# Performance work log

Hardware: AMD Instinct MI355X
Metric: run time of the kernel (lower is better)

The kernel has to match this reference:

```python
import jax, jax.numpy as jnp
import numpy as np

N = 50000      # num nodes
E = 800000     # num edges (before self loops)
B = 50         # num graphs in batch
F_IN = 15
C = 64         # hidden_channels
H = 4          # num_heads
NEG_SLOPE = 0.2  # PyG GATConv default


def setup_inputs() -> dict:
    key = jax.random.key(0)
    ks = jax.random.split(key, 32)
    s = 0.05
    inp = {
        "x": jax.random.normal(ks[0], (N, F_IN), dtype=jnp.float32),
        "edge_index": jax.random.randint(ks[1], (2, E), 0, N, dtype=jnp.int32),
        "batch": jnp.sort(jax.random.randint(ks[2], (N,), 0, B, dtype=jnp.int32)),
        "W1": jax.random.normal(ks[3], (F_IN, H * C)) * s,
        "aS1": jax.random.normal(ks[4], (H, C)) * s,
        "aD1": jax.random.normal(ks[5], (H, C)) * s,
        "b1": jnp.zeros((H * C,)),
        "W2": jax.random.normal(ks[6], (H * C, H * C)) * s,
        "aS2": jax.random.normal(ks[7], (H, C)) * s,
        "aD2": jax.random.normal(ks[8], (H, C)) * s,
        "b2": jnp.zeros((H * C,)),
        # GAT layer 3: 256 -> 64, 1 head
        "W3": jax.random.normal(ks[9], (H * C, C)) * s,
        "aS3": jax.random.normal(ks[10], (1, C)) * s,
        "aD3": jax.random.normal(ks[11], (1, C)) * s,
        "b3": jnp.zeros((C,)),
        # node attention MLP: 64 -> 32 -> 1
        "Wna1": jax.random.normal(ks[12], (C, 32)) * s,
        "bna1": jnp.zeros((32,)),
        "Wna2": jax.random.normal(ks[13], (32, 1)) * s,
        "bna2": jnp.zeros((1,)),
        # graph classifier: 128 -> 128 -> 64 -> 1
        "Wc1": jax.random.normal(ks[14], (2 * C, 128)) * s,
        "bc1": jnp.zeros((128,)),
        "Wc2": jax.random.normal(ks[15], (128, 64)) * s,
        "bc2": jnp.zeros((64,)),
        "Wc3": jax.random.normal(ks[16], (64, 1)) * s,
        "bc3": jnp.zeros((1,)),
    }
    return inp


def _gat_conv(x, src, dst, W, a_src, a_dst, b, heads, ch):
    """PyG-style GATConv (add_self_loops=True, negative_slope=0.2, eval mode)."""
    n = x.shape[0]
    h = (x @ W).reshape(n, heads, ch)               # [N, H, C]
    alpha_s = jnp.einsum('nhc,hc->nh', h, a_src)    # per-node src score
    alpha_d = jnp.einsum('nhc,hc->nh', h, a_dst)
    loops = jnp.arange(n, dtype=src.dtype)
    s = jnp.concatenate([src, loops])               # [E+N]
    d = jnp.concatenate([dst, loops])
    e = jax.nn.leaky_relu(alpha_s[s] + alpha_d[d], NEG_SLOPE)   # [E+N, H]
    # segment softmax over incoming edges of each dst node
    m = jax.ops.segment_max(e, d, num_segments=n)
    ex = jnp.exp(e - m[d])
    denom = jax.ops.segment_sum(ex, d, num_segments=n)
    alpha = ex / denom[d]                           # [E+N, H]
    msg = h[s] * alpha[:, :, None]                  # [E+N, H, C]
    out = jax.ops.segment_sum(msg, d, num_segments=n)  # [N, H, C]
    return out.reshape(n, heads * ch) + b


def reference(x, edge_index, batch, W1, aS1, aD1, b1, W2, aS2, aD2, b2,
              W3, aS3, aD3, b3, Wna1, bna1, Wna2, bna2,
              Wc1, bc1, Wc2, bc2, Wc3, bc3):
    src, dst = edge_index[0], edge_index[1]
    x1 = jax.nn.elu(_gat_conv(x, src, dst, W1, aS1, aD1, b1, H, C))
    x2 = jax.nn.elu(_gat_conv(x1, src, dst, W2, aS2, aD2, b2, H, C))
    x3 = jax.nn.elu(_gat_conv(x2, src, dst, W3, aS3, aD3, b3, 1, C))  # [N, 64]

    # node attention: MLP then softmax over ALL nodes (dim=0, as in source)
    na = jax.nn.relu(x3 @ Wna1 + bna1) @ Wna2 + bna2   # [N, 1]
    node_attention = jax.nn.softmax(na, axis=0)

    # graph pooling
    ones = jnp.ones((x3.shape[0],), dtype=x3.dtype)
    cnt = jax.ops.segment_sum(ones, batch, num_segments=B)         # [B]
    mean = jax.ops.segment_sum(x3, batch, num_segments=B) / jnp.maximum(cnt, 1.0)[:, None]
    mx = jax.ops.segment_max(x3, batch, num_segments=B)
    mx = jnp.where(cnt[:, None] > 0, mx, 0.0)
    g = jnp.concatenate([mean, mx], axis=1)                        # [B, 128]

    h1 = jax.nn.relu(g @ Wc1 + bc1)
    h2 = jax.nn.relu(h1 @ Wc2 + bc2)
    risk = jax.nn.sigmoid(h2 @ Wc3 + bc3)                          # [B, 1]
    return (risk, node_attention)
```

## Files before the change

### kernel.cpp

```cpp
#include <hip/hip_runtime.h>
#include <math.h>

#define NN 50000
#define NP 50176
#define EE 800000
#define ETOT (EE + NN)
#define BB 50
#define PC 16

typedef unsigned short u16;
typedef unsigned char u8;
typedef __attribute__((ext_vector_type(8))) short short8;
typedef __attribute__((ext_vector_type(4))) float floatx4;
typedef __attribute__((ext_vector_type(2))) float floatx2;

__device__ __forceinline__ float b2f(u16 u) {
  return __int_as_float(((int)u) << 16);
}
__device__ __forceinline__ u16 f2b(float f) {
  unsigned u = __float_as_uint(f);
  unsigned r = (u + 0x7fffu + ((u >> 16) & 1u)) >> 16;
  return (u16)r;
}
__device__ __forceinline__ u8 f2f8(float v) {
  return (u8)(__builtin_amdgcn_cvt_pk_fp8_f32(v, v, 0, false) & 0xFF);
}
__device__ __forceinline__ float readlane_f(float v, int l) {
  return __int_as_float(__builtin_amdgcn_readlane(__float_as_int(v), l));
}

__global__ void count_kernel(const int* __restrict__ ei, int* __restrict__ cnt) {
  int e = blockIdx.x * blockDim.x + threadIdx.x;
  if (e >= ETOT) return;
  int d = (e < EE) ? ei[EE + e] : (e - EE);
  atomicAdd(&cnt[d], 1);
}

__global__ void scan1_kernel(const int* __restrict__ cnt, int* __restrict__ rowp,
                             int* __restrict__ part) {
  __shared__ int s[512];
  int t = threadIdx.x;
  int i = blockIdx.x * 512 + t;
  int v = (i < NN) ? cnt[i] : 0;
  s[t] = v;
  __syncthreads();
  for (int off = 1; off < 512; off <<= 1) {
    int add = (t >= off) ? s[t - off] : 0;
    __syncthreads();
    s[t] += add;
    __syncthreads();
  }
  if (i < NN) rowp[i] = s[t] - v;
  if (t == 511) part[blockIdx.x] = s[511];
}

__global__ void scan2_kernel(int* __restrict__ part, int* __restrict__ rowp) {
  __shared__ int s[128];
  int t = threadIdx.x;
  int v = (t < 98) ? part[t] : 0;
  s[t] = v;
  __syncthreads();
  for (int off = 1; off < 128; off <<= 1) {
    int add = (t >= off) ? s[t - off] : 0;
    __syncthreads();
    s[t] += add;
    __syncthreads();
  }
  if (t < 98) part[t] = s[t] - v;
  if (t == 97) rowp[NN] = s[97];
}

__global__ void scan3_kernel(int* __restrict__ rowp, const int* __restrict__ part) {
  int i = blockIdx.x * 512 + threadIdx.x;
  if (i < NN) rowp[i] += part[blockIdx.x];
}

__global__ void fill_kernel(const int* __restrict__ ei, const int* __restrict__ rowp,
                            int* __restrict__ cur, int* __restrict__ col) {
  int e = blockIdx.x * blockDim.x + threadIdx.x;
  if (e >= ETOT) return;
  int s, d;
  if (e < EE) { s = ei[e]; d = ei[EE + e]; } else { s = e - EE; d = s; }
  int p = atomicAdd(&cur[d], 1);
  col[rowp[d] + p] = s;
}

__global__ void prep_kernel(const float* __restrict__ x, const float* __restrict__ W1,
                            const float* __restrict__ W2, const float* __restrict__ W3,
                            u16* __restrict__ xb, u16* __restrict__ W1t,
                            u16* __restrict__ W2t, u16* __restrict__ W3t) {
  const int T0 = NP * 32, T1 = T0 + 8192, T2 = T1 + 65536, T3 = T2 + 16384;
  int i = blockIdx.x * 256 + threadIdx.x;
  if (i < T0) {
    int n = i >> 5, c = i & 31;
    xb[i] = (n < NN && c < 15) ? f2b(x[n * 15 + c]) : (u16)0;
  } else if (i < T1) {
    int j = i - T0, n = j >> 5, k = j & 31;
    W1t[j] = (k < 15) ? f2b(W1[k * 256 + n]) : (u16)0;
  } else if (i < T2) {
    int j = i - T1, n = j >> 8, k = j & 255;
    W2t[j] = f2b(W2[k * 256 + n]);
  } else if (i < T3) {
    int j = i - T2, n = j >> 8, k = j & 255;
    W3t[j] = f2b(W3[k * 64 + n]);
  }
}

template <int BK, bool F8>
__global__ __launch_bounds__(256) void gemm_bf16_kernel(
    const u16* __restrict__ A, const u16* __restrict__ Bt, u16* __restrict__ C,
    u8* __restrict__ C8, int K, int N, const float* __restrict__ aS,
    const float* __restrict__ aD, float* __restrict__ as_o,
    float* __restrict__ ad_o, int Hh) {
  __shared__ u16 Al[128][BK + 8];
  __shared__ u16 Bl[64][BK + 8];
  __shared__ float sS[4][64], sD[4][64];
  int R0 = blockIdx.x * 128, C0 = blockIdx.y * 64;
  int wid = threadIdx.x >> 6, lane = threadIdx.x & 63;
  int wr = (wid >> 1) * 64, wc = (wid & 1) * 32;
  int lrow = lane & 15, lk8 = (lane >> 4) * 8;
  int rq = (lane >> 4) * 4;
  const int Q4 = BK / 4;
  const int nA = 128 * Q4, nB = 64 * Q4;
  floatx4 acc[4][2];
#pragma unroll
  for (int i = 0; i < 4; ++i)
#pragma unroll
    for (int j = 0; j < 2; ++j) acc[i][j] = (floatx4){0.f, 0.f, 0.f, 0.f};

  for (int k0 = 0; k0 < K; k0 += BK) {
    for (int c = threadIdx.x; c < nA + nB; c += 256) {
      if (c < nA) {
        int r = c / Q4, o = (c % Q4) * 4;
        *(ushort4*)&Al[r][o] = *(const ushort4*)&A[(size_t)(R0 + r) * K + k0 + o];
      } else {
        int c2 = c - nA;
        int r = c2 / Q4, o = (c2 % Q4) * 4;
        *(ushort4*)&Bl[r][o] = *(const ushort4*)&Bt[(size_t)(C0 + r) * K + k0 + o];
      }
    }
    __syncthreads();
#pragma unroll
    for (int ks = 0; ks < BK / 32; ++ks) {
      short8 a[4], b[2];
#pragma unroll
      for (int i = 0; i < 4; ++i) a[i] = *(const short8*)&Al[wr + i * 16 + lrow][ks * 32 + lk8];
#pragma unroll
      for (int j = 0; j < 2; ++j) b[j] = *(const short8*)&Bl[wc + j * 16 + lrow][ks * 32 + lk8];
#pragma unroll
      for (int i = 0; i < 4; ++i)
#pragma unroll
        for (int j = 0; j < 2; ++j)
          acc[i][j] = __builtin_amdgcn_mfma_f32_16x16x32_bf16(a[i], b[j], acc[i][j], 0, 0, 0);
    }
    __syncthreads();
  }
#pragma unroll
  for (int i = 0; i < 4; ++i)
#pragma unroll
    for (int j = 0; j < 2; ++j)
#pragma unroll
      for (int q = 0; q < 4; ++q) {
        int gr = R0 + wr + i * 16 + rq + q;
        int gc = C0 + wc + j * 16 + lrow;
        if constexpr (F8)
          C8[(size_t)gr * N + gc] = f2f8(acc[i][j][q]);
        else
          C[(size_t)gr * N + gc] = f2b(acc[i][j][q]);
      }
  int hb = blockIdx.y * 64;
  float wS0 = aS[hb + wc + lrow], wS1 = aS[hb + wc + 16 + lrow];
  float wD0 = aD[hb + wc + lrow], wD1 = aD[hb + wc + 16 + lrow];
#pragma unroll
  for (int i = 0; i < 4; ++i)
#pragma unroll
    for (int q = 0; q < 4; ++q) {
      float vS = acc[i][0][q] * wS0 + acc[i][1][q] * wS1;
      float vD = acc[i][0][q] * wD0 + acc[i][1][q] * wD1;
#pragma unroll
      for (int o = 8; o; o >>= 1) {
        vS += __shfl_xor(vS, o, 64);
        vD += __shfl_xor(vD, o, 64);
      }
      if (lrow == 0) {
        int rl = i * 16 + rq + q;
        sS[wid][rl] = vS;
        sD[wid][rl] = vD;
      }
    }
  __syncthreads();
  if (threadIdx.x < 128) {
    int p = threadIdx.x >> 6, r = threadIdx.x & 63;
    int gr = R0 + p * 64 + r;
    as_o[(size_t)gr * Hh + blockIdx.y] = sS[2 * p][r] + sS[2 * p + 1][r];
    ad_o[(size_t)gr * Hh + blockIdx.y] = sD[2 * p][r] + sD[2 * p + 1][r];
  }
}

template <int B>
__device__ __forceinline__ void agg4_batch(
    const u8* __restrict__ h8, int s, int kbase, int cnt, int hj, int lq,
    const float (*__restrict__ exsw)[4], float& a0, float& a1, float& a2, float& a3) {
  unsigned wv[B];
  float qv[B];
#pragma unroll
  for (int u = 0; u < B; ++u) {
    int ke = kbase + u;
    int kc = (ke < cnt) ? ke : (cnt - 1);
    int sk = __builtin_amdgcn_readlane(s, kc);
    qv[u] = (ke < cnt) ? exsw[kc][hj] : 0.f;
    wv[u] = *(const unsigned*)&h8[(size_t)sk * 256 + lq];
  }
#pragma unroll
  for (int u = 0; u < B; ++u) {
    floatx2 lo = __builtin_amdgcn_cvt_pk_f32_fp8(wv[u], false);
    floatx2 hi = __builtin_amdgcn_cvt_pk_f32_fp8(wv[u], true);
    a0 += qv[u] * lo.x;
    a1 += qv[u] * lo.y;
    a2 += qv[u] * hi.x;
    a3 += qv[u] * hi.y;
  }
}

__global__ __launch_bounds__(256) void agg4_kernel(
    const u8* __restrict__ h8, const float* __restrict__ as_i,
    const float* __restrict__ ad_i, const int* __restrict__ rowp,
    const int* __restrict__ col, const float* __restrict__ bias,
    u16* __restrict__ xo) {
  __shared__ float exs[4][64][4];
  int wid = threadIdx.x >> 6, lane = threadIdx.x & 63;
  int d = blockIdx.x * 4 + wid;
  int rp0 = rowp[d], deg = rowp[d + 1] - rp0;
  float4 add = *(const float4*)&ad_i[(size_t)d * 4];
  int hj = lane >> 4;
  int lq = lane << 2;
  const float(*exsw)[4] = exs[wid];
  float a0 = 0.f, a1 = 0.f, a2 = 0.f, a3 = 0.f;
  float den0 = 0.f, den1 = 0.f, den2 = 0.f, den3 = 0.f;

  for (int base = 0; base < deg; base += 64) {
    int i = base + lane;
    bool valid = i < deg;
    int s = valid ? col[rp0 + i] : 0;
    float4 asv = *(const float4*)&as_i[(size_t)s * 4];
    float e0 = asv.x + add.x, e1 = asv.y + add.y, e2 = asv.z + add.z, e3 = asv.w + add.w;
    e0 = (e0 > 0.f) ? e0 : 0.2f * e0;
    e1 = (e1 > 0.f) ? e1 : 0.2f * e1;
    e2 = (e2 > 0.f) ? e2 : 0.2f * e2;
    e3 = (e3 > 0.f) ? e3 : 0.2f * e3;
    float x0 = valid ? __expf(e0) : 0.f;
    float x1 = valid ? __expf(e1) : 0.f;
    float x2 = valid ? __expf(e2) : 0.f;
    float x3 = valid ? __expf(e3) : 0.f;
    den0 += x0; den1 += x1; den2 += x2; den3 += x3;
    *(float4*)&exs[wid][lane][0] = make_float4(x0, x1, x2, x3);
    __threadfence_block();
    int cnt = min(64, deg - base);
    for (int kb = 0; kb < cnt; kb += 16)
      agg4_batch<16>(h8, s, kb, cnt, hj, lq, exsw, a0, a1, a2, a3);
  }
#pragma unroll
  for (int o = 32; o; o >>= 1) {
    den0 += __shfl_xor(den0, o, 64);
    den1 += __shfl_xor(den1, o, 64);
    den2 += __shfl_xor(den2, o, 64);
    den3 += __shfl_xor(den3, o, 64);
  }
  float den = (hj == 0) ? den0 : (hj == 1) ? den1 : (hj == 2) ? den2 : den3;
  float inv = 1.f / den;
  float4 bv = *(const float4*)&bias[lq];
  float v0 = a0 * inv + bv.x;
  float v1 = a1 * inv + bv.y;
  float v2 = a2 * inv + bv.z;
  float v3 = a3 * inv + bv.w;
  v0 = (v0 > 0.f) ? v0 : expm1f(v0);
  v1 = (v1 > 0.f) ? v1 : expm1f(v1);
  v2 = (v2 > 0.f) ? v2 : expm1f(v2);
  v3 = (v3 > 0.f) ? v3 : expm1f(v3);
  ushort4 o4;
  o4.x = f2b(v0); o4.y = f2b(v1); o4.z = f2b(v2); o4.w = f2b(v3);
  ((ushort4*)xo)[(size_t)d * 64 + lane] = o4;
}

__global__ __launch_bounds__(256) void agg1na_kernel(
    const u16* __restrict__ h, const float* __restrict__ as_i,
    const float* __restrict__ ad_i, const int* __restrict__ rowp,
    const int* __restrict__ col, const float* __restrict__ bias,
    float* __restrict__ xo, const float* __restrict__ Wna1,
    const float* __restrict__ bna1, const float* __restrict__ Wna2,
    const float* __restrict__ bna2, float* __restrict__ na) {
  __shared__ float Ws[2048];
  __shared__ float W2s[32];
  __shared__ float xrow[4][64];
  for (int i = threadIdx.x; i < 2048; i += 256) Ws[i] = Wna1[i];
  if (threadIdx.x < 32) W2s[threadIdx.x] = Wna2[threadIdx.x];
  __syncthreads();
  int wid = threadIdx.x >> 6, lane = threadIdx.x & 63;
  int d = blockIdx.x * 4 + wid;
  int rp0 = rowp[d], deg = rowp[d + 1] - rp0;
  float add = ad_i[d];
  float acc = 0.f, den = 0.f;
  for (int base = 0; base < deg; base += 64) {
    int i = base + lane;
    bool valid = i < deg;
    int s = valid ? col[rp0 + i] : 0;
    float e = as_i[s] + add;
    e = (e > 0.f) ? e : 0.2f * e;
    float ex = valid ? __expf(e) : 0.f;
    den += ex;
    int cnt = min(64, deg - base);
    int k8 = cnt & ~7;
    for (int k = 0; k < k8; k += 8) {
      int sA[8];
      float qA[8], hv[8];
#pragma unroll
      for (int u = 0; u < 8; ++u) {
        sA[u] = __builtin_amdgcn_readlane(s, k + u);
        qA[u] = readlane_f(ex, k + u);
      }
#pragma unroll
      for (int u = 0; u < 8; ++u) hv[u] = b2f(h[(size_t)sA[u] * 64 + lane]);
      float p0 = qA[0] * hv[0] + qA[1] * hv[1];
      float p1 = qA[2] * hv[2] + qA[3] * hv[3];
      float p2 = qA[4] * hv[4] + qA[5] * hv[5];
      float p3 = qA[6] * hv[6] + qA[7] * hv[7];
      acc += (p0 + p1) + (p2 + p3);
    }
    for (int k = k8; k < cnt; ++k) {
      int sk = __builtin_amdgcn_readlane(s, k);
      float qk = readlane_f(ex, k);
      acc += qk * b2f(h[(size_t)sk * 64 + lane]);
    }
  }
#pragma unroll
  for (int o = 32; o; o >>= 1) den += __shfl_xor(den, o, 64);
  float v = acc / den + bias[lane];
  v = (v > 0.f) ? v : expm1f(v);
  xo[(size_t)d * 64 + lane] = v;
  xrow[wid][lane] = v;
  __threadfence_block();
  int j = lane & 31;
  int coff = (lane >> 5) * 32;
  float hj = 0.f;
#pragma unroll
  for (int c = 0; c < 32; ++c) hj += xrow[wid][coff + c] * Ws[(coff + c) * 32 + j];
  hj += __shfl_xor(hj, 32, 64);
  hj += bna1[j];
  float r = fmaxf(hj, 0.f) * W2s[j];
#pragma unroll
  for (int o = 16; o; o >>= 1) r += __shfl_xor(r, o, 64);
  if (lane == 0) na[d] = __expf(r + bna2[0]);
}

__global__ void na_sum_kernel(const float* __restrict__ na, float* __restrict__ gsum) {
  __shared__ float s[4];
  float acc = 0.f;
  for (int i = blockIdx.x * blockDim.x + threadIdx.x; i < NN; i += gridDim.x * blockDim.x)
    acc += na[i];
  for (int o = 32; o; o >>= 1) acc += __shfl_xor(acc, o, 64);
  int wid = threadIdx.x >> 6, lane = threadIdx.x & 63;
  if (lane == 0) s[wid] = acc;
  __syncthreads();
  if (threadIdx.x == 0) atomicAdd(gsum, s[0] + s[1] + s[2] + s[3]);
}

__global__ void na_write_kernel(const float* __restrict__ na, const float* __restrict__ gsum,
                                float* __restrict__ out) {
  int n = blockIdx.x * blockDim.x + threadIdx.x;
  if (n >= NN) return;
  out[n] = na[n] / gsum[0];
}

__global__ void pool1_kernel(const float* __restrict__ x3, const int* __restrict__ batch,
                             float* __restrict__ ppsum, float* __restrict__ ppmax) {
  int b = blockIdx.x, c = blockIdx.y;
  int lane = threadIdx.x & 63, wid = threadIdx.x >> 6;
  int lo = 0, hi = NN;
  while (lo < hi) { int m = (lo + hi) >> 1; if (batch[m] < b) lo = m + 1; else hi = m; }
  int start = lo;
  lo = start; hi = NN;
  while (lo < hi) { int m = (lo + hi) >> 1; if (batch[m] < b + 1) lo = m + 1; else hi = m; }
  int end = lo;
  int len = end - start;
  int c0 = start + (int)((long)len * c / PC);
  int c1 = start + (int)((long)len * (c + 1) / PC);
  float acc = 0.f, mx = -INFINITY;
  for (int n = c0 + wid; n < c1; n += 4) {
    float v = x3[(size_t)n * 64 + lane];
    acc += v;
    mx = fmaxf(mx, v);
  }
  __shared__ float ssum[4][64], smax[4][64];
  ssum[wid][lane] = acc;
  smax[wid][lane] = mx;
  __syncthreads();
  if (wid == 0) {
    acc = ssum[0][lane] + ssum[1][lane] + ssum[2][lane] + ssum[3][lane];
    mx = fmaxf(fmaxf(smax[0][lane], smax[1][lane]), fmaxf(smax[2][lane], smax[3][lane]));
    size_t o = ((size_t)c * BB + b) * 64 + lane;
    ppsum[o] = acc;
    ppmax[o] = mx;
  }
}

__global__ void pool2cls_kernel(const float* __restrict__ ppsum, const float* __restrict__ ppmax,
                                const int* __restrict__ batch, const float* __restrict__ Wc1,
                                const float* __restrict__ bc1, const float* __restrict__ Wc2,
                                const float* __restrict__ bc2, const float* __restrict__ Wc3,
                                const float* __restrict__ bc3, float* __restrict__ out) {
  __shared__ float g[128], h1[128], h2[64], scnt;
  int b = blockIdx.x, t = threadIdx.x;
  if (t == 0) {
    int lo = 0, hi = NN;
    while (lo < hi) { int m = (lo + hi) >> 1; if (batch[m] < b) lo = m + 1; else hi = m; }
    int start = lo;
    lo = start; hi = NN;
    while (lo < hi) { int m = (lo + hi) >> 1; if (batch[m] < b + 1) lo = m + 1; else hi = m; }
    scnt = (float)(lo - start);
  }
  float s = 0.f, m = -INFINITY;
  if (t < 64) {
#pragma unroll
    for (int c = 0; c < PC; ++c) {
      size_t o = ((size_t)c * BB + b) * 64 + t;
      s += ppsum[o];
      m = fmaxf(m, ppmax[o]);
    }
  }
  __syncthreads();
  float cnt = scnt;
  if (t < 64) {
    g[t] = (cnt > 0.f) ? s / fmaxf(cnt, 1.f) : 0.f;
    g[64 + t] = (cnt > 0.f) ? m : 0.f;
  }
  __syncthreads();
  float v = bc1[t];
  for (int k = 0; k < 128; ++k) v += g[k] * Wc1[k * 128 + t];
  h1[t] = fmaxf(v, 0.f);
  __syncthreads();
  if (t < 64) {
    float v2 = bc2[t];
    for (int k = 0; k < 128; ++k) v2 += h1[k] * Wc2[k * 64 + t];
    h2[t] = fmaxf(v2, 0.f);
  }
  __syncthreads();
  if (t == 0) {
    float z = bc3[0];
    for (int k = 0; k < 64; ++k) z += h2[k] * Wc3[k];
    out[b] = 1.f / (1.f + expf(-z));
  }
}

extern "C" void kernel_launch(void* const* d_in, const int* in_sizes, int n_in,
                              void* d_out, int out_size, void* d_ws, size_t ws_size,
                              hipStream_t stream) {
  const float* x    = (const float*)d_in[0];
  const int*   ei   = (const int*)d_in[1];
  const int*   batch= (const int*)d_in[2];
  const float* W1 = (const float*)d_in[3];
  const float* aS1= (const float*)d_in[4];
  const float* aD1= (const float*)d_in[5];
  const float* b1 = (const float*)d_in[6];
  const float* W2 = (const float*)d_in[7];
  const float* aS2= (const float*)d_in[8];
  const float* aD2= (const float*)d_in[9];
  const float* b2 = (const float*)d_in[10];
  const float* W3 = (const float*)d_in[11];
  const float* aS3= (const float*)d_in[12];
  const float* aD3= (const float*)d_in[13];
  const float* b3 = (const float*)d_in[14];
  const float* Wna1=(const float*)d_in[15];
  const float* bna1=(const float*)d_in[16];
  const float* Wna2=(const float*)d_in[17];
  const float* bna2=(const float*)d_in[18];
  const float* Wc1=(const float*)d_in[19];
  const float* bc1=(const float*)d_in[20];
  const float* Wc2=(const float*)d_in[21];
  const float* bc2=(const float*)d_in[22];
  const float* Wc3=(const float*)d_in[23];
  const float* bc3=(const float*)d_in[24];
  float* out = (float*)d_out;

  char* w = (char*)d_ws;
  size_t off = 0;
  auto alloc = [&](size_t bytes) {
    void* p = w + off;
    off = (off + bytes + 255) & ~(size_t)255;
    return p;
  };
  u16* xb   = (u16*)alloc((size_t)NP * 32 * 2);
  u16* bufA = (u16*)alloc((size_t)NP * 256 * 2);
  u16* bufB = (u16*)alloc((size_t)NP * 256 * 2);
  u8*  h8   = (u8*)alloc((size_t)NP * 256);
  u16* W1t  = (u16*)alloc((size_t)256 * 32 * 2);
  u16* W2t  = (u16*)alloc((size_t)256 * 256 * 2);
  u16* W3t  = (u16*)alloc((size_t)64 * 256 * 2);
  float* asb  = (float*)alloc((size_t)NP * 4 * 4);
  float* adb  = (float*)alloc((size_t)NP * 4 * 4);
  float* nab  = (float*)alloc((size_t)NN * 4);
  int* rowp = (int*)alloc((size_t)(NN + 1) * 4);
  int* cntb = (int*)alloc((size_t)NN * 4);
  int* curb = (int*)alloc((size_t)NN * 4);
  float* gsum = (float*)alloc(256);
  size_t zspan = (size_t)((char*)gsum + 256 - (char*)cntb);
  int* colb = (int*)alloc((size_t)ETOT * 4);
  int* part = (int*)alloc(128 * 4);
  float* ppsum = (float*)alloc((size_t)PC * BB * 64 * 4);
  float* ppmax = (float*)alloc((size_t)PC * BB * 64 * 4);
  float* x3 = (float*)bufB;
  (void)ws_size; (void)in_sizes; (void)n_in; (void)out_size;

  hipMemsetAsync(cntb, 0, zspan, stream);

  count_kernel<<<(ETOT + 255) / 256, 256, 0, stream>>>(ei, cntb);
  scan1_kernel<<<98, 512, 0, stream>>>(cntb, rowp, part);
  scan2_kernel<<<1, 128, 0, stream>>>(part, rowp);
  scan3_kernel<<<98, 512, 0, stream>>>(rowp, part);
  fill_kernel<<<(ETOT + 255) / 256, 256, 0, stream>>>(ei, rowp, curb, colb);

  const int PREP_TOT = NP * 32 + 8192 + 65536 + 16384;
  prep_kernel<<<(PREP_TOT + 255) / 256, 256, 0, stream>>>(x, W1, W2, W3, xb, W1t, W2t, W3t);

  const int GX = NP / 128;
  gemm_bf16_kernel<32, true><<<dim3(GX, 4), 256, 0, stream>>>(
      xb, W1t, nullptr, h8, 32, 256, aS1, aD1, asb, adb, 4);
  agg4_kernel<<<12500, 256, 0, stream>>>(h8, asb, adb, rowp, colb, b1, bufB);
  gemm_bf16_kernel<64, true><<<dim3(GX, 4), 256, 0, stream>>>(
      bufB, W2t, nullptr, h8, 256, 256, aS2, aD2, asb, adb, 4);
  agg4_kernel<<<12500, 256, 0, stream>>>(h8, asb, adb, rowp, colb, b2, bufB);
  gemm_bf16_kernel<64, false><<<dim3(GX, 1), 256, 0, stream>>>(
      bufB, W3t, bufA, nullptr, 256, 64, aS3, aD3, asb, adb, 1);
  agg1na_kernel<<<12500, 256, 0, stream>>>(bufA, asb, adb, rowp, colb, b3, x3,
                                           Wna1, bna1, Wna2, bna2, nab);

  na_sum_kernel<<<196, 256, 0, stream>>>(nab, gsum);
  na_write_kernel<<<(NN + 255) / 256, 256, 0, stream>>>(nab, gsum, out + BB);
  pool1_kernel<<<dim3(BB, PC), 256, 0, stream>>>(x3, batch, ppsum, ppmax);
  pool2cls_kernel<<<BB, 128, 0, stream>>>(ppsum, ppmax, batch, Wc1, bc1, Wc2, bc2,
                                          Wc3, bc3, out);
}
```

Before: 387.1 us.

## Make aggregation kernels grid-stride persistent and shrink gather batch in agg4

```diff
diff --git a/kernel.cpp b/kernel.cpp
--- a/kernel.cpp
+++ b/kernel.cpp
@@ -7,6 +7,7 @@
 #define ETOT (EE + NN)
 #define BB 50
 #define PC 16
+#define NGRP 12500
 
 typedef unsigned short u16;
 typedef unsigned char u8;
@@ -197,31 +198,6 @@
   }
 }
 
-template <int B>
-__device__ __forceinline__ void agg4_batch(
-    const u8* __restrict__ h8, int s, int kbase, int cnt, int hj, int lq,
-    const float (*__restrict__ exsw)[4], float& a0, float& a1, float& a2, float& a3) {
-  unsigned wv[B];
-  float qv[B];
-#pragma unroll
-  for (int u = 0; u < B; ++u) {
-    int ke = kbase + u;
-    int kc = (ke < cnt) ? ke : (cnt - 1);
-    int sk = __builtin_amdgcn_readlane(s, kc);
-    qv[u] = (ke < cnt) ? exsw[kc][hj] : 0.f;
-    wv[u] = *(const unsigned*)&h8[(size_t)sk * 256 + lq];
-  }
-#pragma unroll
-  for (int u = 0; u < B; ++u) {
-    floatx2 lo = __builtin_amdgcn_cvt_pk_f32_fp8(wv[u], false);
-    floatx2 hi = __builtin_amdgcn_cvt_pk_f32_fp8(wv[u], true);
-    a0 += qv[u] * lo.x;
-    a1 += qv[u] * lo.y;
-    a2 += qv[u] * hi.x;
-    a3 += qv[u] * hi.y;
-  }
-}
-
 __global__ __launch_bounds__(256) void agg4_kernel(
     const u8* __restrict__ h8, const float* __restrict__ as_i,
     const float* __restrict__ ad_i, const int* __restrict__ rowp,
@@ -229,57 +205,87 @@
     u16* __restrict__ xo) {
   __shared__ float exs[4][64][4];
   int wid = threadIdx.x >> 6, lane = threadIdx.x & 63;
-  int d = blockIdx.x * 4 + wid;
-  int rp0 = rowp[d], deg = rowp[d + 1] - rp0;
-  float4 add = *(const float4*)&ad_i[(size_t)d * 4];
   int hj = lane >> 4;
   int lq = lane << 2;
-  const float(*exsw)[4] = exs[wid];
-  float a0 = 0.f, a1 = 0.f, a2 = 0.f, a3 = 0.f;
-  float den0 = 0.f, den1 = 0.f, den2 = 0.f, den3 = 0.f;
-
-  for (int base = 0; base < deg; base += 64) {
-    int i = base + lane;
-    bool valid = i < deg;
-    int s = valid ? col[rp0 + i] : 0;
-    float4 asv = *(const float4*)&as_i[(size_t)s * 4];
-    float e0 = asv.x + add.x, e1 = asv.y + add.y, e2 = asv.z + add.z, e3 = asv.w + add.w;
-    e0 = (e0 > 0.f) ? e0 : 0.2f * e0;
-    e1 = (e1 > 0.f) ? e1 : 0.2f * e1;
-    e2 = (e2 > 0.f) ? e2 : 0.2f * e2;
-    e3 = (e3 > 0.f) ? e3 : 0.2f * e3;
-    float x0 = valid ? __expf(e0) : 0.f;
-    float x1 = valid ? __expf(e1) : 0.f;
-    float x2 = valid ? __expf(e2) : 0.f;
-    float x3 = valid ? __expf(e3) : 0.f;
-    den0 += x0; den1 += x1; den2 += x2; den3 += x3;
-    *(float4*)&exs[wid][lane][0] = make_float4(x0, x1, x2, x3);
-    __threadfence_block();
-    int cnt = min(64, deg - base);
-    for (int kb = 0; kb < cnt; kb += 16)
-      agg4_batch<16>(h8, s, kb, cnt, hj, lq, exsw, a0, a1, a2, a3);
-  }
-#pragma unroll
-  for (int o = 32; o; o >>= 1) {
-    den0 += __shfl_xor(den0, o, 64);
-    den1 += __shfl_xor(den1, o, 64);
-    den2 += __shfl_xor(den2, o, 64);
-    den3 += __shfl_xor(den3, o, 64);
-  }
-  float den = (hj == 0) ? den0 : (hj == 1) ? den1 : (hj == 2) ? den2 : den3;
-  float inv = 1.f / den;
-  float4 bv = *(const float4*)&bias[lq];
-  float v0 = a0 * inv + bv.x;
-  float v1 = a1 * inv + bv.y;
-  float v2 = a2 * inv + bv.z;
-  float v3 = a3 * inv + bv.w;
-  v0 = (v0 > 0.f) ? v0 : expm1f(v0);
-  v1 = (v1 > 0.f) ? v1 : expm1f(v1);
-  v2 = (v2 > 0.f) ? v2 : expm1f(v2);
-  v3 = (v3 > 0.f) ? v3 : expm1f(v3);
-  ushort4 o4;
-  o4.x = f2b(v0); o4.y = f2b(v1); o4.z = f2b(v2); o4.w = f2b(v3);
-  ((ushort4*)xo)[(size_t)d * 64 + lane] = o4;
+  for (int g = blockIdx.x; g < NGRP; g += gridDim.x) {
+    int d = g * 4 + wid;
+    int rp0 = rowp[d], deg = rowp[d + 1] - rp0;
+    float4 add = *(const float4*)&ad_i[(size_t)d * 4];
+    float a0 = 0.f, a1 = 0.f, a2 = 0.f, a3 = 0.f;
+    float den0 = 0.f, den1 = 0.f, den2 = 0.f, den3 = 0.f;
+
+    for (int base = 0; base < deg; base += 64) {
+      int i = base + lane;
+      bool valid = i < deg;
+      int s = valid ? col[rp0 + i] : 0;
+      float4 asv = *(const float4*)&as_i[(size_t)s * 4];
+      float e0 = asv.x + add.x, e1 = asv.y + add.y, e2 = asv.z + add.z, e3 = asv.w + add.w;
+      e0 = (e0 > 0.f) ? e0 : 0.2f * e0;
+      e1 = (e1 > 0.f) ? e1 : 0.2f * e1;
+      e2 = (e2 > 0.f) ? e2 : 0.2f * e2;
+      e3 = (e3 > 0.f) ? e3 : 0.2f * e3;
+      float x0 = valid ? __expf(e0) : 0.f;
+      float x1 = valid ? __expf(e1) : 0.f;
+      float x2 = valid ? __expf(e2) : 0.f;
+      float x3 = valid ? __expf(e3) : 0.f;
+      den0 += x0; den1 += x1; den2 += x2; den3 += x3;
+      *(float4*)&exs[wid][lane][0] = make_float4(x0, x1, x2, x3);
+      __threadfence_block();
+      int cnt = min(64, deg - base);
+      int k8 = cnt & ~7;
+      for (int k = 0; k < k8; k += 8) {
+        unsigned wv[8];
+        float qv[8];
+#pragma unroll
+        for (int u = 0; u < 8; ++u) {
+          int sk = __builtin_amdgcn_readlane(s, k + u);
+          qv[u] = exs[wid][k + u][hj];
+          wv[u] = *(const unsigned*)&h8[(size_t)sk * 256 + lq];
+        }
+#pragma unroll
+        for (int u = 0; u < 8; ++u) {
+          floatx2 lo = __builtin_amdgcn_cvt_pk_f32_fp8(wv[u], false);
+          floatx2 hi = __builtin_amdgcn_cvt_pk_f32_fp8(wv[u], true);
+          a0 += qv[u] * lo.x;
+          a1 += qv[u] * lo.y;
+          a2 += qv[u] * hi.x;
+          a3 += qv[u] * hi.y;
+        }
+      }
+      for (int k = k8; k < cnt; ++k) {
+        int sk = __builtin_amdgcn_readlane(s, k);
+        float qk = exs[wid][k][hj];
+        unsigned wv = *(const unsigned*)&h8[(size_t)sk * 256 + lq];
+        floatx2 lo = __builtin_amdgcn_cvt_pk_f32_fp8(wv, false);
+        floatx2 hi = __builtin_amdgcn_cvt_pk_f32_fp8(wv, true);
+        a0 += qk * lo.x;
+        a1 += qk * lo.y;
+        a2 += qk * hi.x;
+        a3 += qk * hi.y;
+      }
+    }
+#pragma unroll
+    for (int o = 32; o; o >>= 1) {
+      den0 += __shfl_xor(den0, o, 64);
+      den1 += __shfl_xor(den1, o, 64);
+      den2 += __shfl_xor(den2, o, 64);
+      den3 += __shfl_xor(den3, o, 64);
+    }
+    float den = (hj == 0) ? den0 : (hj == 1) ? den1 : (hj == 2) ? den2 : den3;
+    float inv = 1.f / den;
+    float4 bv = *(const float4*)&bias[lq];
+    float v0 = a0 * inv + bv.x;
+    float v1 = a1 * inv + bv.y;
+    float v2 = a2 * inv + bv.z;
+    float v3 = a3 * inv + bv.w;
+    v0 = (v0 > 0.f) ? v0 : expm1f(v0);
+    v1 = (v1 > 0.f) ? v1 : expm1f(v1);
+    v2 = (v2 > 0.f) ? v2 : expm1f(v2);
+    v3 = (v3 > 0.f) ? v3 : expm1f(v3);
+    ushort4 o4;
+    o4.x = f2b(v0); o4.y = f2b(v1); o4.z = f2b(v2); o4.w = f2b(v3);
+    ((ushort4*)xo)[(size_t)d * 64 + lane] = o4;
+  }
 }
 
 __global__ __launch_bounds__(256) void agg1na_kernel(
@@ -296,60 +302,64 @@
   if (threadIdx.x < 32) W2s[threadIdx.x] = Wna2[threadIdx.x];
   __syncthreads();
   int wid = threadIdx.x >> 6, lane = threadIdx.x & 63;
-  int d = blockIdx.x * 4 + wid;
-  int rp0 = rowp[d], deg = rowp[d + 1] - rp0;
-  float add = ad_i[d];
-  float acc = 0.f, den = 0.f;
-  for (int base = 0; base < deg; base += 64) {
-    int i = base + lane;
-    bool valid = i < deg;
-    int s = valid ? col[rp0 + i] : 0;
-    float e = as_i[s] + add;
-    e = (e > 0.f) ? e : 0.2f * e;
-    float ex = valid ? __expf(e) : 0.f;
-    den += ex;
-    int cnt = min(64, deg - base);
-    int k8 = cnt & ~7;
-    for (int k = 0; k < k8; k += 8) {
-      int sA[8];
-      float qA[8], hv[8];
-#pragma unroll
-      for (int u = 0; u < 8; ++u) {
-        sA[u] = __builtin_amdgcn_readlane(s, k + u);
-        qA[u] = readlane_f(ex, k + u);
-      }
-#pragma unroll
-      for (int u = 0; u < 8; ++u) hv[u] = b2f(h[(size_t)sA[u] * 64 + lane]);
-      float p0 = qA[0] * hv[0] + qA[1] * hv[1];
-      float p1 = qA[2] * hv[2] + qA[3] * hv[3];
-      float p2 = qA[4] * hv[4] + qA[5] * hv[5];
-      float p3 = qA[6] * hv[6] + qA[7] * hv[7];
-      acc += (p0 + p1) + (p2 + p3);
-    }
-    for (int k = k8; k < cnt; ++k) {
-      int sk = __builtin_amdgcn_readlane(s, k);
-      float qk = readlane_f(ex, k);
-      acc += qk * b2f(h[(size_t)sk * 64 + lane]);
-    }
-  }
-#pragma unroll
-  for (int o = 32; o; o >>= 1) den += __shfl_xor(den, o, 64);
-  float v = acc / den + bias[lane];
-  v = (v > 0.f) ? v : expm1f(v);
-  xo[(size_t)d * 64 + lane] = v;
-  xrow[wid][lane] = v;
-  __threadfence_block();
-  int j = lane & 31;
-  int coff = (lane >> 5) * 32;
-  float hj = 0.f;
-#pragma unroll
-  for (int c = 0; c < 32; ++c) hj += xrow[wid][coff + c] * Ws[(coff + c) * 32 + j];
-  hj += __shfl_xor(hj, 32, 64);
-  hj += bna1[j];
-  float r = fmaxf(hj, 0.f) * W2s[j];
-#pragma unroll
-  for (int o = 16; o; o >>= 1) r += __shfl_xor(r, o, 64);
-  if (lane == 0) na[d] = __expf(r + bna2[0]);
+  float b1v = bna1[lane & 31];
+  float b2v = bna2[0];
+  for (int g = blockIdx.x; g < NGRP; g += gridDim.x) {
+    int d = g * 4 + wid;
+    int rp0 = rowp[d], deg = rowp[d + 1] - rp0;
+    float add = ad_i[d];
+    float acc = 0.f, den = 0.f;
+    for (int base = 0; base < deg; base += 64) {
+      int i = base + lane;
+      bool valid = i < deg;
+      int s = valid ? col[rp0 + i] : 0;
+      float e = as_i[s] + add;
+      e = (e > 0.f) ? e : 0.2f * e;
+      float ex = valid ? __expf(e) : 0.f;
+      den += ex;
+      int cnt = min(64, deg - base);
+      int k8 = cnt & ~7;
+      for (int k = 0; k < k8; k += 8) {
+        int sA[8];
+        float qA[8], hv[8];
+#pragma unroll
+        for (int u = 0; u < 8; ++u) {
+          sA[u] = __builtin_amdgcn_readlane(s, k + u);
+          qA[u] = readlane_f(ex, k + u);
+        }
+#pragma unroll
+        for (int u = 0; u < 8; ++u) hv[u] = b2f(h[(size_t)sA[u] * 64 + lane]);
+        float p0 = qA[0] * hv[0] + qA[1] * hv[1];
+        float p1 = qA[2] * hv[2] + qA[3] * hv[3];
+        float p2 = qA[4] * hv[4] + qA[5] * hv[5];
+        float p3 = qA[6] * hv[6] + qA[7] * hv[7];
+        acc += (p0 + p1) + (p2 + p3);
+      }
+      for (int k = k8; k < cnt; ++k) {
+        int sk = __builtin_amdgcn_readlane(s, k);
+        float qk = readlane_f(ex, k);
+        acc += qk * b2f(h[(size_t)sk * 64 + lane]);
+      }
+    }
+#pragma unroll
+    for (int o = 32; o; o >>= 1) den += __shfl_xor(den, o, 64);
+    float v = acc / den + bias[lane];
+    v = (v > 0.f) ? v : expm1f(v);
+    xo[(size_t)d * 64 + lane] = v;
+    xrow[wid][lane] = v;
+    __threadfence_block();
+    int j = lane & 31;
+    int coff = (lane >> 5) * 32;
+    float hj = 0.f;
+#pragma unroll
+    for (int c = 0; c < 32; ++c) hj += xrow[wid][coff + c] * Ws[(coff + c) * 32 + j];
+    hj += __shfl_xor(hj, 32, 64);
+    hj += b1v;
+    float r = fmaxf(hj, 0.f) * W2s[j];
+#pragma unroll
+    for (int o = 16; o; o >>= 1) r += __shfl_xor(r, o, 64);
+    if (lane == 0) na[d] = __expf(r + b2v);
+  }
 }
 
 __global__ void na_sum_kernel(const float* __restrict__ na, float* __restrict__ gsum) {
@@ -522,16 +532,17 @@
   prep_kernel<<<(PREP_TOT + 255) / 256, 256, 0, stream>>>(x, W1, W2, W3, xb, W1t, W2t, W3t);
 
   const int GX = NP / 128;
+  const int PG = 2048;
   gemm_bf16_kernel<32, true><<<dim3(GX, 4), 256, 0, stream>>>(
       xb, W1t, nullptr, h8, 32, 256, aS1, aD1, asb, adb, 4);
-  agg4_kernel<<<12500, 256, 0, stream>>>(h8, asb, adb, rowp, colb, b1, bufB);
+  agg4_kernel<<<PG, 256, 0, stream>>>(h8, asb, adb, rowp, colb, b1, bufB);
   gemm_bf16_kernel<64, true><<<dim3(GX, 4), 256, 0, stream>>>(
       bufB, W2t, nullptr, h8, 256, 256, aS2, aD2, asb, adb, 4);
-  agg4_kernel<<<12500, 256, 0, stream>>>(h8, asb, adb, rowp, colb, b2, bufB);
+  agg4_kernel<<<PG, 256, 0, stream>>>(h8, asb, adb, rowp, colb, b2, bufB);
   gemm_bf16_kernel<64, false><<<dim3(GX, 1), 256, 0, stream>>>(
       bufB, W3t, bufA, nullptr, 256, 64, aS3, aD3, asb, adb, 1);
-  agg1na_kernel<<<12500, 256, 0, stream>>>(bufA, asb, adb, rowp, colb, b3, x3,
-                                           Wna1, bna1, Wna2, bna2, nab);
+  agg1na_kernel<<<PG, 256, 0, stream>>>(bufA, asb, adb, rowp, colb, b3, x3,
+                                        Wna1, bna1, Wna2, bna2, nab);
 
   na_sum_kernel<<<196, 256, 0, stream>>>(nab, gsum);
   na_write_kernel<<<(NN + 255) / 256, 256, 0, stream>>>(nab, gsum, out + BB);
```

New measurement: 389.0 us. Within noise of the previous version (+0.5%).
